# Kernel tuning notes

Measured on AMD Instinct MI355X. Metric: run time of the kernel, lower is better.

The kernel has to match this reference:

```python
import jax, jax.numpy as jnp
import numpy as np

B, C, D, T = 64, 1024, 32, 32
F4 = C // 4
GLOBAL_MARGIN = 0.2
MAX_VIOLATION = True
EPS = 1e-8


def setup_inputs() -> dict:
    key = jax.random.key(0)
    k = jax.random.split(key, 8)
    videos = jax.random.normal(k[0], (B, C, D, T), jnp.float32)
    sentences = jax.random.normal(k[1], (B, C), jnp.float32)
    lam = jnp.full((1,), 0.3, jnp.float32)
    mask = jnp.ones((B, D, T), jnp.int32)
    iou_maps = jax.random.uniform(k[2], (D * T, D * T), dtype=jnp.float32)
    lim = float(np.sqrt(6.0 / (C + F4)))  # xavier_uniform for Linear(C, C//4)
    W_v = jax.random.uniform(k[3], (4, C, F4), jnp.float32, -lim, lim)
    b_v = jnp.zeros((4, F4), jnp.float32)
    W_s = jax.random.uniform(k[4], (4, C, F4), jnp.float32, -lim, lim)
    b_s = jnp.zeros((4, F4), jnp.float32)
    return dict(videos=videos, sentences=sentences, lam=lam, mask=mask,
                iou_maps=iou_maps, valid_num=50,
                W_v=W_v, b_v=b_v, W_s=W_s, b_s=b_s)


def _forward(videos, sentences, W_v, b_v, W_s, b_s, lam, mask, iou_maps, valid_num):
    b, c, d, t = videos.shape
    # per-sample channel-mean centering
    videos = videos - jnp.mean(videos, axis=1, keepdims=True)
    sentences = sentences - jnp.mean(sentences, axis=1, keepdims=True)
    # 4-way linear projections, concatenated back along channel dim
    v = jnp.transpose(videos, (0, 2, 3, 1))                      # [b,d,t,c]
    v_cat = (jnp.einsum('bdtc,kcf->bkfdt', v, W_v)
             + b_v[None, :, :, None, None]).reshape(b, c, d, t)  # [b,c,d,t]
    s_cat = (jnp.einsum('bc,kcf->bkf', sentences, W_s) + b_s[None]).reshape(b, c)
    # cosine similarity over channel dim, vectorized over the batch loop
    vn = v_cat / jnp.maximum(jnp.linalg.norm(v_cat, axis=1, keepdims=True), EPS)
    sn = s_cat / jnp.maximum(jnp.linalg.norm(s_cat, axis=1, keepdims=True), EPS)
    sim = jnp.einsum('bcdt,sc->sbdt', vn, sn)                    # [s,b,d,t]
    sim = jnp.where(mask[None] == 0, -jnp.inf, sim)
    positive_map = sim[jnp.arange(b), jnp.arange(b)]             # [b,d,t]
    # top-k proposals + soft-NMS suppression (get_video_score_nms)
    flat = sim.reshape(b, b, d * t)
    vals, idx = jax.lax.top_k(flat, valid_num)                   # [s,b,v]
    iou_sub = iou_maps[idx[..., :, None], idx[..., None, :]]     # [s,b,v,v]
    tril = jnp.tril(jnp.ones((valid_num, valid_num), vals.dtype), -1)
    penalty = jnp.einsum('sblk,lk->sbk', iou_sub * iou_sub, tril)
    w = jnp.exp(-penalty / lam[0])                               # gaussian soft-NMS weight
    scores = jnp.mean(vals * w, axis=-1)                         # [s,b]
    # margin-based contrastive loss on the b x b score matrix
    diag = jnp.diagonal(scores)
    cost_s = jnp.clip(GLOBAL_MARGIN + scores - diag[:, None], 0.0)
    cost_im = jnp.clip(GLOBAL_MARGIN + scores - diag[None, :], 0.0)
    eye = jnp.eye(b, dtype=bool)
    cost_s = jnp.where(eye, 0.0, cost_s)
    cost_im = jnp.where(eye, 0.0, cost_im)
    if MAX_VIOLATION:
        cost_s = cost_s.max(axis=1)
        cost_im = cost_im.max(axis=0)
    loss = cost_s.sum() / b + cost_im.sum() / b
    return loss, positive_map


def reference(videos, sentences, lam, mask, iou_maps, valid_num, W_v, b_v, W_s, b_s):
    return _forward(videos, sentences, W_v, b_v, W_s, b_s, lam, mask, iou_maps, valid_num)
```

## Files before the change

### kernel.cpp

```cpp
#include <hip/hip_runtime.h>
#include <cstdint>
#include <cstddef>

#define CDIM  1024
#define DTDIM 1024
#define MDIM  65536
#define BDIM  64
#define VNUM  50

typedef __attribute__((ext_vector_type(8))) short bf16x8;
typedef __attribute__((ext_vector_type(4))) float f32x4;

__device__ __forceinline__ float bf2f(unsigned int u16) {
  return __uint_as_float(u16 << 16);
}
__device__ __forceinline__ unsigned short f2bf(float x) {
  unsigned int u = __float_as_uint(x);
  u += 0x7fffu + ((u >> 16) & 1u);
  return (unsigned short)(u >> 16);
}

__device__ __forceinline__ void gload16(const void* g, void* l) {
  __builtin_amdgcn_global_load_lds((const __attribute__((address_space(1))) void*)g,
                                   (__attribute__((address_space(3))) void*)l,
                                   16, 0, 0);
}

__global__ void k_transpose_videos(const float* __restrict__ vid,
                                   unsigned short* __restrict__ At,
                                   float* __restrict__ vsums) {
  __shared__ float t[64][65];
  const int tid = threadIdx.x;
  const int dt0 = blockIdx.x * 64, c0 = blockIdx.y * 64, b = blockIdx.z;
  const int lc = tid >> 4;
  const int l4 = (tid & 15) * 4;
  const float* src = vid + ((size_t)b * CDIM + c0) * DTDIM + dt0;
#pragma unroll
  for (int p = 0; p < 4; p++) {
    const int c = p * 16 + lc;
    const float4 f = *reinterpret_cast<const float4*>(&src[(size_t)c * DTDIM + l4]);
    t[c][l4 + 0] = f.x; t[c][l4 + 1] = f.y; t[c][l4 + 2] = f.z; t[c][l4 + 3] = f.w;
  }
  __syncthreads();
  const int dr = tid >> 5;
  const int cl = tid & 31;
  unsigned int* dstbase = reinterpret_cast<unsigned int*>(
      At + ((size_t)(b * DTDIM + dt0)) * CDIM + c0);
#pragma unroll
  for (int p = 0; p < 8; p++) {
    const int dt = p * 8 + dr;
    const float a0 = t[2 * cl][dt], a1 = t[2 * cl + 1][dt];
    const unsigned int u = (unsigned int)f2bf(a0) | ((unsigned int)f2bf(a1) << 16);
    dstbase[(size_t)dt * 512 + cl] = u;
    float s = a0 + a1;
    s += __shfl_xor(s, 1);  s += __shfl_xor(s, 2);  s += __shfl_xor(s, 4);
    s += __shfl_xor(s, 8);  s += __shfl_xor(s, 16);
    if (cl == 0) atomicAdd(&vsums[(size_t)b * DTDIM + dt0 + dt], s);
  }
}

__global__ void k_transpose_W(const float* __restrict__ W,
                              unsigned short* __restrict__ Wt) {
  __shared__ float t[32][33];
  const int tx = threadIdx.x & 31, ty = threadIdx.x >> 5;
  const int f0 = blockIdx.x * 32, c0 = blockIdx.y * 32, kb = blockIdx.z;
  const float* src = W + ((size_t)kb * CDIM + c0) * 256 + f0;
#pragma unroll
  for (int i = 0; i < 4; i++) {
    const int cl = ty + i * 8;
    t[cl][tx] = src[(size_t)cl * 256 + tx];
  }
  __syncthreads();
  unsigned short* dst = Wt + ((size_t)(kb * 256 + f0)) * CDIM + c0;
#pragma unroll
  for (int i = 0; i < 4; i++) {
    const int fl = ty + i * 8;
    dst[(size_t)fl * CDIM + tx] = f2bf(t[tx][fl]);
  }
}

__global__ void k_row_sums(const unsigned short* __restrict__ A,
                           float* __restrict__ out, int nrows) {
  const int wave = threadIdx.x >> 6, lane = threadIdx.x & 63;
  const int row = blockIdx.x * 4 + wave;
  if (row >= nrows) return;
  const unsigned short* r = A + (size_t)row * 1024;
  float s = 0.f;
#pragma unroll
  for (int h = 0; h < 2; h++) {
    const uint4 u = *reinterpret_cast<const uint4*>(r + h * 512 + lane * 8);
    s += bf2f(u.x & 0xffffu) + bf2f(u.x >> 16);
    s += bf2f(u.y & 0xffffu) + bf2f(u.y >> 16);
    s += bf2f(u.z & 0xffffu) + bf2f(u.z >> 16);
    s += bf2f(u.w & 0xffffu) + bf2f(u.w >> 16);
  }
#pragma unroll
  for (int o = 32; o; o >>= 1) s += __shfl_down(s, o);
  if (lane == 0) out[row] = s;
}

__global__ void k_scat(const float* __restrict__ sent, const float* __restrict__ Ws,
                       const float* __restrict__ bs, unsigned short* __restrict__ scat,
                       float* __restrict__ snorm2) {
  const int s = blockIdx.x, j = blockIdx.y, tid = threadIdx.x;
  __shared__ float sc[1024];
  __shared__ float red[4];
  float p = 0.f;
#pragma unroll
  for (int q = 0; q < 4; q++) {
    const float x = sent[(size_t)s * 1024 + tid + q * 256];
    sc[tid + q * 256] = x;
    p += x;
  }
#pragma unroll
  for (int o = 32; o; o >>= 1) p += __shfl_down(p, o);
  const int wave = tid >> 6, lane = tid & 63;
  if (lane == 0) red[wave] = p;
  __syncthreads();
  const float mean = (red[0] + red[1] + red[2] + red[3]) * (1.f / 1024.f);
  float acc = 0.f;
  const float* W = Ws + ((size_t)j * 1024) * 256 + tid;
  for (int c = 0; c < 1024; c++) acc += (sc[c] - mean) * W[(size_t)c * 256];
  const int n = j * 256 + tid;
  const float val = acc + bs[n];
  scat[(size_t)s * 1024 + n] = f2bf(val);
  float v2 = val * val;
#pragma unroll
  for (int o = 32; o; o >>= 1) v2 += __shfl_down(v2, o);
  if (lane == 0) atomicAdd(&snorm2[s], v2);
}

__global__ __launch_bounds__(256, 2) void k_gemm_fused(
    const unsigned short* __restrict__ At, const unsigned short* __restrict__ Wt,
    const float* __restrict__ vsums, const float* __restrict__ csW,
    const float* __restrict__ bv, const unsigned short* __restrict__ scat,
    const float* __restrict__ snorm2, const int* __restrict__ mask,
    float* __restrict__ sim, float* __restrict__ pm) {
  __shared__ alignas(16) char smem[32768 + 16384 + 256 + 1024];
  unsigned short* sAB   = (unsigned short*)smem;
  unsigned short* vtile = (unsigned short*)smem;
  unsigned short* stile = (unsigned short*)(smem + 32768);
  float* invSnLds       = (float*)(smem + 49152);
  float* vnLds          = (float*)(smem + 49152 + 256);

  const int tid = threadIdx.x;
  const int wave = tid >> 6, lane = tid & 63;
  const int quad = lane >> 4, l16 = lane & 15;
  const int m0 = blockIdx.x * 128;
  const int wm = (wave & 1) * 64, wn = (wave >> 1) * 64;

  if (tid < 64) invSnLds[tid] = 1.f / fmaxf(sqrtf(snorm2[tid]), 1e-8f);

  f32x4 acc2[4][2];
#pragma unroll
  for (int i = 0; i < 4; i++)
#pragma unroll
    for (int j = 0; j < 2; j++) acc2[i][j] = f32x4{0.f, 0.f, 0.f, 0.f};
  float ss[4][4];
#pragma unroll
  for (int i = 0; i < 4; i++)
#pragma unroll
    for (int rr = 0; rr < 4; rr++) ss[i][rr] = 0.f;

  const float inv1024 = 1.f / 1024.f;

  for (int nt = 0; nt < 8; ++nt) {
    const int n0 = nt * 128;

#pragma unroll
    for (int ii = 0; ii < 4; ii++) {
      const int srow = (ii * 4 + wave) * 4 + (lane >> 4);
      const int g = (lane & 15) ^ (srow & 15);
      gload16(scat + (size_t)srow * 1024 + n0 + g * 8,
              stile + (ii * 4 + wave) * 512);
    }

    f32x4 acc[4][4];
#pragma unroll
    for (int i = 0; i < 4; i++)
#pragma unroll
      for (int j = 0; j < 4; j++) acc[i][j] = f32x4{0.f, 0.f, 0.f, 0.f};

    for (int kt = 0; kt < 16; ++kt) {
      const int koff = kt * 64;
#pragma unroll
      for (int ii = 0; ii < 4; ii++) {
        const int r = (ii * 4 + wave) * 8 + (lane >> 3);
        const int g = (lane & 7) ^ (r & 7);
        gload16(At + (size_t)(m0 + r) * CDIM + koff + g * 8,
                sAB + (ii * 4 + wave) * 512);
        gload16(Wt + (size_t)(n0 + r) * CDIM + koff + g * 8,
                sAB + 8192 + (ii * 4 + wave) * 512);
      }
      __syncthreads();
#pragma unroll
      for (int ks = 0; ks < 2; ks++) {
        const int slot = ((ks * 4 + quad) ^ (l16 & 7)) * 8;
        bf16x8 aF[4], bF[4];
#pragma unroll
        for (int i = 0; i < 4; i++)
          aF[i] = *reinterpret_cast<const bf16x8*>(&sAB[(wm + i * 16 + l16) * 64 + slot]);
#pragma unroll
        for (int j = 0; j < 4; j++)
          bF[j] = *reinterpret_cast<const bf16x8*>(&sAB[8192 + (wn + j * 16 + l16) * 64 + slot]);
#pragma unroll
        for (int i = 0; i < 4; i++)
#pragma unroll
          for (int j = 0; j < 4; j++)
            acc[i][j] = __builtin_amdgcn_mfma_f32_16x16x32_bf16(aF[i], bF[j], acc[i][j], 0, 0, 0);
      }
      __syncthreads();
    }

#pragma unroll
    for (int i = 0; i < 4; i++) {
      const int rbase = wm + i * 16 + quad * 4;
      const float4 vs = *reinterpret_cast<const float4*>(&vsums[m0 + rbase]);
      const float mu[4] = {vs.x * inv1024, vs.y * inv1024, vs.z * inv1024, vs.w * inv1024};
#pragma unroll
      for (int j = 0; j < 4; j++) {
        const int c = wn + j * 16 + l16;
        const float cs = csW[n0 + c];
        const float bb = bv[n0 + c];
#pragma unroll
        for (int rr = 0; rr < 4; rr++) {
          const int m = rbase + rr;
          const float val = acc[i][j][rr] - mu[rr] * cs + bb;
          ss[i][rr] += val * val;
          const int slot = (c >> 3) ^ (m & 15);
          vtile[m * 128 + slot * 8 + (c & 7)] = f2bf(val);
        }
      }
    }
    __syncthreads();

#pragma unroll
    for (int ks2 = 0; ks2 < 4; ks2++) {
      const int slot = ((ks2 * 4 + quad) ^ l16) * 8;
      bf16x8 a2[4], b2[2];
#pragma unroll
      for (int i2 = 0; i2 < 4; i2++)
        a2[i2] = *reinterpret_cast<const bf16x8*>(&stile[(i2 * 16 + l16) * 128 + slot]);
#pragma unroll
      for (int j2 = 0; j2 < 2; j2++)
        b2[j2] = *reinterpret_cast<const bf16x8*>(&vtile[(wave * 32 + j2 * 16 + l16) * 128 + slot]);
#pragma unroll
      for (int i2 = 0; i2 < 4; i2++)
#pragma unroll
        for (int j2 = 0; j2 < 2; j2++)
          acc2[i2][j2] = __builtin_amdgcn_mfma_f32_16x16x32_bf16(a2[i2], b2[j2], acc2[i2][j2], 0, 0, 0);
    }
    __syncthreads();
  }

#pragma unroll
  for (int i = 0; i < 4; i++)
#pragma unroll
    for (int rr = 0; rr < 4; rr++) {
      float v = ss[i][rr];
      v += __shfl_xor(v, 1); v += __shfl_xor(v, 2);
      v += __shfl_xor(v, 4); v += __shfl_xor(v, 8);
      if (l16 == 0) vnLds[(wave >> 1) * 128 + wm + i * 16 + quad * 4 + rr] = v;
    }
  __syncthreads();

  const int b0 = m0 >> 10;
#pragma unroll
  for (int j2 = 0; j2 < 2; j2++) {
    const int ml = wave * 32 + j2 * 16 + l16;
    const float nv = vnLds[ml] + vnLds[128 + ml];
    const float invVn = 1.f / fmaxf(sqrtf(nv), 1e-8f);
    const int mk = mask[m0 + ml];
#pragma unroll
    for (int i2 = 0; i2 < 4; i2++) {
#pragma unroll
      for (int reg = 0; reg < 4; reg++) {
        const int s = i2 * 16 + quad * 4 + reg;
        float val = acc2[i2][j2][reg] * invVn * invSnLds[s];
        if (mk == 0) val = -__builtin_inff();
        sim[(size_t)s * MDIM + m0 + ml] = val;
        if (s == b0) pm[m0 + ml] = val;
      }
    }
  }
}

__global__ void k_topk(const float* __restrict__ sim, const float* __restrict__ iou,
                       const float* __restrict__ lam, float* __restrict__ scores) {
  const int wave = threadIdx.x >> 6, lane = threadIdx.x & 63;
  const int sb = blockIdx.x * 4 + wave;
  const int s = sb >> 6, b = sb & 63;
  __shared__ float tvs[4][VNUM];
  __shared__ int tis[4][VNUM];

  const float* row = sim + (size_t)s * MDIM + (size_t)b * 1024;
  float v[16];
#pragma unroll
  for (int j = 0; j < 16; j++) v[j] = row[j * 64 + lane];

  for (int k = 0; k < VNUM; k++) {
    float bv = v[0]; int bj = 0;
#pragma unroll
    for (int j = 1; j < 16; j++)
      if (v[j] > bv) { bv = v[j]; bj = j; }
    int bidx = bj * 64 + lane;
#pragma unroll
    for (int o = 1; o < 64; o <<= 1) {
      const float ov = __shfl_xor(bv, o);
      const int oi = __shfl_xor(bidx, o);
      if (ov > bv || (ov == bv && oi < bidx)) { bv = ov; bidx = oi; }
    }
    if (lane == 0) { tvs[wave][k] = bv; tis[wave][k] = bidx; }
    const int wj = bidx >> 6;
    const bool mine = (bidx & 63) == lane;
#pragma unroll
    for (int j = 0; j < 16; j++)
      if (mine && wj == j) v[j] = -__builtin_inff();
  }
  __syncthreads();

  float contrib = 0.f;
  if (lane < VNUM) {
    const int myidx = tis[wave][lane];
    float pen = 0.f;
    for (int l = lane + 1; l < VNUM; l++) {
      const float u = iou[(size_t)tis[wave][l] * 1024 + myidx];
      pen += u * u;
    }
    contrib = tvs[wave][lane] * expf(-pen / lam[0]);
  }
#pragma unroll
  for (int o = 32; o; o >>= 1) contrib += __shfl_down(contrib, o);
  if (lane == 0) scores[s * 64 + b] = contrib * (1.f / VNUM);
}

__global__ void k_loss(const float* __restrict__ scores, float* __restrict__ out) {
  __shared__ float S[64 * 64];
  __shared__ float diag[64];
  __shared__ float rmax[64], cmax[64];
  const int tid = threadIdx.x;
#pragma unroll
  for (int q = 0; q < 16; q++) S[tid + q * 256] = scores[tid + q * 256];
  __syncthreads();
  if (tid < 64) diag[tid] = S[tid * 64 + tid];
  __syncthreads();
  if (tid < 64) {
    float rm = 0.f, cm = 0.f;
    for (int x = 0; x < 64; x++) {
      if (x != tid) {
        const float cs = 0.2f + S[tid * 64 + x] - diag[tid];
        rm = fmaxf(rm, fmaxf(cs, 0.f));
        const float ci = 0.2f + S[x * 64 + tid] - diag[tid];
        cm = fmaxf(cm, fmaxf(ci, 0.f));
      }
    }
    rmax[tid] = rm; cmax[tid] = cm;
  }
  __syncthreads();
  if (tid == 0) {
    float L = 0.f;
    for (int t = 0; t < 64; t++) L += rmax[t] + cmax[t];
    out[0] = L * (1.f / 64.f);
  }
}

extern "C" void kernel_launch(void* const* d_in, const int* in_sizes, int n_in,
                              void* d_out, int out_size, void* d_ws, size_t ws_size,
                              hipStream_t stream) {
  (void)in_sizes; (void)n_in; (void)out_size; (void)ws_size;
  const float* videos = (const float*)d_in[0];
  const float* sent   = (const float*)d_in[1];
  const float* lam    = (const float*)d_in[2];
  const int*   mask   = (const int*)d_in[3];
  const float* iou    = (const float*)d_in[4];
  const float* W_v    = (const float*)d_in[6];
  const float* b_v    = (const float*)d_in[7];
  const float* W_s    = (const float*)d_in[8];
  const float* b_s    = (const float*)d_in[9];
  float* out = (float*)d_out;

  char* ws = (char*)d_ws;
  unsigned short* At   = (unsigned short*)(ws + 0);
  float* sim           = (float*)(ws + 134217728);
  unsigned short* Wt   = (unsigned short*)(ws + 150994944);
  unsigned short* scat = (unsigned short*)(ws + 153092096);
  float* vsums         = (float*)(ws + 153223168);
  float* snorm2        = (float*)(ws + 153485312);
  float* csW           = (float*)(ws + 153485568);
  float* scores        = (float*)(ws + 153489664);

  hipMemsetAsync(vsums, 0, 262144 + 256, stream);

  k_transpose_videos<<<dim3(16, 16, 64), 256, 0, stream>>>(videos, At, vsums);
  k_transpose_W<<<dim3(8, 32, 4), 256, 0, stream>>>(W_v, Wt);
  k_row_sums<<<256, 256, 0, stream>>>(Wt, csW, 1024);
  k_scat<<<dim3(64, 4), 256, 0, stream>>>(sent, W_s, b_s, scat, snorm2);
  k_gemm_fused<<<dim3(512), 256, 0, stream>>>(At, Wt, vsums, csW, b_v, scat,
                                              snorm2, mask, sim, out + 1);
  k_topk<<<dim3(1024), 256, 0, stream>>>(sim, iou, lam, scores);
  k_loss<<<1, 256, 0, stream>>>(scores, out);
}
```

Baseline: 725.3 us.

## Double-buffer GEMM tiles with 512-thread 256-row blocks in fused projection kernel

The fused projection/similarity GEMM now uses 512-thread blocks, each covering 256 video rows instead of 128. A/B k-tiles are double-buffered in LDS so the next tile's global-to-LDS loads overlap the current tile's MFMAs, with explicit vmcnt waits and barriers, and wave priority is raised during compute. This targets exposed load latency and the per-iteration sync stalls of the previous single-buffered loop. In exchange LDS use grows to about 114 KB per block and the grid halves to 256 blocks, which lowers occupancy and may leave some CUs idle.

```diff
diff --git a/kernel.cpp b/kernel.cpp
--- a/kernel.cpp
+++ b/kernel.cpp
@@ -130,24 +130,26 @@
   if (lane == 0) atomicAdd(&snorm2[s], v2);
 }
 
-__global__ __launch_bounds__(256, 2) void k_gemm_fused(
+__global__ __launch_bounds__(512, 2) void k_gemm_fused(
     const unsigned short* __restrict__ At, const unsigned short* __restrict__ Wt,
     const float* __restrict__ vsums, const float* __restrict__ csW,
     const float* __restrict__ bv, const unsigned short* __restrict__ scat,
     const float* __restrict__ snorm2, const int* __restrict__ mask,
     float* __restrict__ sim, float* __restrict__ pm) {
-  __shared__ alignas(16) char smem[32768 + 16384 + 256 + 1024];
-  unsigned short* sAB   = (unsigned short*)smem;
+  __shared__ alignas(16) char smem[116992];
+  unsigned short* sA    = (unsigned short*)smem;
+  unsigned short* sB    = (unsigned short*)(smem + 65536);
+  unsigned short* stile = (unsigned short*)(smem + 98304);
+  float* invSnLds       = (float*)(smem + 114688);
+  float* vnLds          = (float*)(smem + 114944);
   unsigned short* vtile = (unsigned short*)smem;
-  unsigned short* stile = (unsigned short*)(smem + 32768);
-  float* invSnLds       = (float*)(smem + 49152);
-  float* vnLds          = (float*)(smem + 49152 + 256);
 
   const int tid = threadIdx.x;
   const int wave = tid >> 6, lane = tid & 63;
   const int quad = lane >> 4, l16 = lane & 15;
-  const int m0 = blockIdx.x * 128;
-  const int wm = (wave & 1) * 64, wn = (wave >> 1) * 64;
+  const int m0 = blockIdx.x * 256;
+  const int wm = (wave & 3) * 64, wn = (wave >> 2) * 64;
+  const int r8 = lane >> 3, g8 = lane & 7;
 
   if (tid < 64) invSnLds[tid] = 1.f / fmaxf(sqrtf(snorm2[tid]), 1e-8f);
 
@@ -164,16 +166,27 @@
 
   const float inv1024 = 1.f / 1024.f;
 
+#pragma unroll 1
   for (int nt = 0; nt < 8; ++nt) {
     const int n0 = nt * 128;
 
-#pragma unroll
-    for (int ii = 0; ii < 4; ii++) {
-      const int srow = (ii * 4 + wave) * 4 + (lane >> 4);
-      const int g = (lane & 15) ^ (srow & 15);
-      gload16(scat + (size_t)srow * 1024 + n0 + g * 8,
-              stile + (ii * 4 + wave) * 512);
-    }
+    auto stage_ab = [&](int buf, int kt) {
+      const int koff = kt * 64;
+      unsigned short* dA = sA + buf * 16384;
+      unsigned short* dB = sB + buf * 8192;
+#pragma unroll
+      for (int ii = 0; ii < 4; ii++) {
+        const int q = ii * 8 + wave;
+        const int r = q * 8 + r8;
+        gload16(At + (size_t)(m0 + r) * CDIM + koff + (g8 ^ r8) * 8, dA + q * 512);
+      }
+#pragma unroll
+      for (int ii = 0; ii < 2; ii++) {
+        const int q = ii * 8 + wave;
+        const int r = q * 8 + r8;
+        gload16(Wt + (size_t)(n0 + r) * CDIM + koff + (g8 ^ r8) * 8, dB + q * 512);
+      }
+    };
 
     f32x4 acc[4][4];
 #pragma unroll
@@ -181,36 +194,54 @@
 #pragma unroll
       for (int j = 0; j < 4; j++) acc[i][j] = f32x4{0.f, 0.f, 0.f, 0.f};
 
-    for (int kt = 0; kt < 16; ++kt) {
-      const int koff = kt * 64;
-#pragma unroll
-      for (int ii = 0; ii < 4; ii++) {
-        const int r = (ii * 4 + wave) * 8 + (lane >> 3);
-        const int g = (lane & 7) ^ (r & 7);
-        gload16(At + (size_t)(m0 + r) * CDIM + koff + g * 8,
-                sAB + (ii * 4 + wave) * 512);
-        gload16(Wt + (size_t)(n0 + r) * CDIM + koff + g * 8,
-                sAB + 8192 + (ii * 4 + wave) * 512);
-      }
-      __syncthreads();
+    auto compute = [&](int buf) {
+      const unsigned short* bA = sA + buf * 16384;
+      const unsigned short* bB = sB + buf * 8192;
+      __builtin_amdgcn_s_setprio(1);
 #pragma unroll
       for (int ks = 0; ks < 2; ks++) {
         const int slot = ((ks * 4 + quad) ^ (l16 & 7)) * 8;
         bf16x8 aF[4], bF[4];
 #pragma unroll
         for (int i = 0; i < 4; i++)
-          aF[i] = *reinterpret_cast<const bf16x8*>(&sAB[(wm + i * 16 + l16) * 64 + slot]);
+          aF[i] = *reinterpret_cast<const bf16x8*>(&bA[(wm + i * 16 + l16) * 64 + slot]);
 #pragma unroll
         for (int j = 0; j < 4; j++)
-          bF[j] = *reinterpret_cast<const bf16x8*>(&sAB[8192 + (wn + j * 16 + l16) * 64 + slot]);
+          bF[j] = *reinterpret_cast<const bf16x8*>(&bB[(wn + j * 16 + l16) * 64 + slot]);
 #pragma unroll
         for (int i = 0; i < 4; i++)
 #pragma unroll
           for (int j = 0; j < 4; j++)
             acc[i][j] = __builtin_amdgcn_mfma_f32_16x16x32_bf16(aF[i], bF[j], acc[i][j], 0, 0, 0);
       }
-      __syncthreads();
-    }
+      __builtin_amdgcn_s_setprio(0);
+    };
+
+#pragma unroll
+    for (int ii = 0; ii < 2; ii++) {
+      const int q = ii * 8 + wave;
+      const int srow = q * 4 + (lane >> 4);
+      const int g = (lane & 15) ^ (srow & 15);
+      gload16(scat + (size_t)srow * 1024 + n0 + g * 8, stile + q * 512);
+    }
+    stage_ab(0, 0);
+
+    int cur = 0;
+#pragma unroll 1
+    for (int kt = 0; kt < 15; ++kt) {
+      stage_ab(cur ^ 1, kt + 1);
+      asm volatile("s_waitcnt vmcnt(6)" ::: "memory");
+      __builtin_amdgcn_s_barrier();
+      asm volatile("" ::: "memory");
+      compute(cur);
+      __builtin_amdgcn_s_barrier();
+      cur ^= 1;
+    }
+    asm volatile("s_waitcnt vmcnt(0)" ::: "memory");
+    __builtin_amdgcn_s_barrier();
+    asm volatile("" ::: "memory");
+    compute(cur);
+    __syncthreads();
 
 #pragma unroll
     for (int i = 0; i < 4; i++) {
@@ -260,7 +291,7 @@
       float v = ss[i][rr];
       v += __shfl_xor(v, 1); v += __shfl_xor(v, 2);
       v += __shfl_xor(v, 4); v += __shfl_xor(v, 8);
-      if (l16 == 0) vnLds[(wave >> 1) * 128 + wm + i * 16 + quad * 4 + rr] = v;
+      if (l16 == 0) vnLds[(wave >> 2) * 256 + wm + i * 16 + quad * 4 + rr] = v;
     }
   __syncthreads();
 
@@ -268,7 +299,7 @@
 #pragma unroll
   for (int j2 = 0; j2 < 2; j2++) {
     const int ml = wave * 32 + j2 * 16 + l16;
-    const float nv = vnLds[ml] + vnLds[128 + ml];
+    const float nv = vnLds[ml] + vnLds[256 + ml];
     const float invVn = 1.f / fmaxf(sqrtf(nv), 1e-8f);
     const int mk = mask[m0 + ml];
 #pragma unroll
@@ -395,7 +426,7 @@
   k_transpose_W<<<dim3(8, 32, 4), 256, 0, stream>>>(W_v, Wt);
   k_row_sums<<<256, 256, 0, stream>>>(Wt, csW, 1024);
   k_scat<<<dim3(64, 4), 256, 0, stream>>>(sent, W_s, b_s, scat, snorm2);
-  k_gemm_fused<<<dim3(512), 256, 0, stream>>>(At, Wt, vsums, csW, b_v, scat,
+  k_gemm_fused<<<dim3(256), 512, 0, stream>>>(At, Wt, vsums, csW, b_v, scat,
                                               snorm2, mask, sim, out + 1);
   k_topk<<<dim3(1024), 256, 0, stream>>>(sim, iou, lam, scores);
   k_loss<<<1, 256, 0, stream>>>(scores, out);
```

Measured after the change: 717.8 us. Within noise of the previous version (-1.0%).
